# Optimization experiments

Measured on AMD Instinct MI355X. Metric: run time of the kernel, lower is better.

Reference implementation:

```python
import jax, jax.numpy as jnp
import numpy as np

N = 16384      # number of nodes (= in_num_dim)
F_DIM = 512    # node feature dim (= in_node_dim)
EMBED = 128    # embed_dim (D1)
OUT = 64       # out_dim (final latent)
E = 524288     # number of edges (avg degree 32)
GAT_SLOPE = 0.5    # GATConv negative_slope
LRELU_SLOPE = 0.01 # F.leaky_relu default on embed


def setup_inputs() -> dict:
    key = jax.random.key(0)
    ks = jax.random.split(key, 10)
    x = jax.random.normal(ks[0], (N, F_DIM), dtype=jnp.float32)
    edge_index = jax.random.randint(ks[1], (2, E), 0, N, dtype=jnp.int64)
    adj = jnp.zeros((1,), dtype=jnp.float32)  # unused by forward (as in source)
    # GATConv params (single head)
    W_gat = jax.random.normal(ks[2], (F_DIM, OUT), dtype=jnp.float32) / np.sqrt(F_DIM)
    att_src = jax.random.normal(ks[3], (OUT,), dtype=jnp.float32) * 0.1
    att_dst = jax.random.normal(ks[4], (OUT,), dtype=jnp.float32) * 0.1
    b_gat = jnp.zeros((OUT,), dtype=jnp.float32)
    # AttributeAE params: dense1 (N -> EMBED), dense2 (EMBED -> OUT)
    W1 = jax.random.normal(ks[5], (N, EMBED), dtype=jnp.float32) / np.sqrt(N)
    b1 = jnp.zeros((EMBED,), dtype=jnp.float32)
    W2 = jax.random.normal(ks[6], (EMBED, OUT), dtype=jnp.float32) / np.sqrt(EMBED)
    b2 = jnp.zeros((OUT,), dtype=jnp.float32)
    return dict(x=x, edge_index=edge_index, adj=adj, W_gat=W_gat,
                att_src=att_src, att_dst=att_dst, b_gat=b_gat,
                W1=W1, b1=b1, W2=W2, b2=b2)


def _gat_conv(x, edge_index, W_gat, att_src, att_dst, b_gat):
    # PyG GATConv, heads=1, with self-loops appended.
    n = x.shape[0]
    loops = jnp.arange(n, dtype=edge_index.dtype)
    src = jnp.concatenate([edge_index[0], loops])  # message sources j
    dst = jnp.concatenate([edge_index[1], loops])  # aggregation targets i
    h = x @ W_gat                                  # [N, OUT]
    a_src = h @ att_src                            # [N]
    a_dst = h @ att_dst                            # [N]
    e = jax.nn.leaky_relu(a_src[src] + a_dst[dst], GAT_SLOPE)  # [E+N]
    # segment softmax over incoming edges of each dst node
    m = jax.ops.segment_max(e, dst, num_segments=n)
    p = jnp.exp(e - m[dst])
    denom = jax.ops.segment_sum(p, dst, num_segments=n)
    alpha = p / denom[dst]
    out = jax.ops.segment_sum(alpha[:, None] * h[src], dst, num_segments=n)
    return out + b_gat


def _forward(x, edge_index, W_gat, att_src, att_dst, b_gat, W1, b1, W2, b2):
    # StructureAE
    embed_x = jax.nn.leaky_relu(
        _gat_conv(x, edge_index, W_gat, att_src, att_dst, b_gat), LRELU_SLOPE)
    A_hat = jax.nn.sigmoid(embed_x @ embed_x.T)          # [N, N]
    # AttributeAE (dropout = 0 -> identity)
    h1 = jax.nn.relu(x.T @ W1 + b1)                      # [F, EMBED]
    h2 = h1 @ W2 + b2                                    # [F, OUT]
    X_hat = embed_x @ h2.T                               # [N, F]
    return A_hat, X_hat


def reference(x, edge_index, adj, W_gat, att_src, att_dst, b_gat, W1, b1, W2, b2):
    # adj is accepted but unused, matching the torch forward signature
    return _forward(x, edge_index, W_gat, att_src, att_dst, b_gat, W1, b1, W2, b2)
```

## Files before the change

### kernel.cpp

```cpp
#include <hip/hip_runtime.h>
#include <hip/hip_bf16.h>

#define NN 16384
#define FD 512
#define EMB 128
#define OD 64
#define NE 524288

typedef __bf16 bf16x8 __attribute__((ext_vector_type(8)));
typedef float f32x4 __attribute__((ext_vector_type(4)));
typedef unsigned short u16;

__device__ inline float bfu2f(u16 u) {
    unsigned int x = (unsigned int)u << 16;
    float f;
    __builtin_memcpy(&f, &x, 4);
    return f;
}

__global__ __launch_bounds__(256) void k_prep(
    const float* __restrict__ x, __hip_bfloat16* __restrict__ xbf,
    const float* __restrict__ Wg, __hip_bfloat16* __restrict__ WgT,
    const int* __restrict__ ei, int* __restrict__ deg,
    const float* __restrict__ W1, float* __restrict__ part) {
    __shared__ float xs[4][64];
    __shared__ float wsh[4][EMB];
    int b = blockIdx.x;
    int t = threadIdx.x;
    if (b < 256) {
        int fb = b & 7, nc = b >> 3;
        int f0 = fb * 64, nb = nc * 512;
        int eb = (t & 15) * 8;
        int fbase = (t >> 4) * 4;
        float acc[4][8] = {};
        for (int n4 = 0; n4 < 512; n4 += 4) {
            { int nn = t >> 6, ff = t & 63;
              xs[nn][ff] = x[(size_t)(nb + n4 + nn) * FD + f0 + ff]; }
#pragma unroll
            for (int j = 0; j < 2; ++j) {
                int idx = t + j * 256;
                wsh[idx >> 7][idx & 127] = W1[(size_t)(nb + n4 + (idx >> 7)) * EMB + (idx & 127)];
            }
            __syncthreads();
#pragma unroll
            for (int nn = 0; nn < 4; ++nn) {
                float xv[4], wv[8];
#pragma unroll
                for (int i = 0; i < 4; ++i) xv[i] = xs[nn][fbase + i];
#pragma unroll
                for (int j = 0; j < 8; ++j) wv[j] = wsh[nn][eb + j];
#pragma unroll
                for (int i = 0; i < 4; ++i)
#pragma unroll
                    for (int j = 0; j < 8; ++j) acc[i][j] += xv[i] * wv[j];
            }
            __syncthreads();
        }
#pragma unroll
        for (int i = 0; i < 4; ++i) {
            float* dst = &part[((size_t)nc * FD + f0 + fbase + i) * EMB + eb];
            *reinterpret_cast<f32x4*>(dst) = *reinterpret_cast<f32x4*>(&acc[i][0]);
            *reinterpret_cast<f32x4*>(dst + 4) = *reinterpret_cast<f32x4*>(&acc[i][4]);
        }
        return;
    }
    b -= 256;
    if (b < NE / 256) {
        int i = b * 256 + t;
        atomicAdd(deg + ei[NE + i], 1);
        return;
    }
    b -= NE / 256;
    if (b < NN * FD / 2048) {
        size_t i = ((size_t)b * 256 + t) * 8;
        float4 v0 = *reinterpret_cast<const float4*>(x + i);
        float4 v1 = *reinterpret_cast<const float4*>(x + i + 4);
        __hip_bfloat16 o[8];
        o[0] = __float2bfloat16(v0.x); o[1] = __float2bfloat16(v0.y);
        o[2] = __float2bfloat16(v0.z); o[3] = __float2bfloat16(v0.w);
        o[4] = __float2bfloat16(v1.x); o[5] = __float2bfloat16(v1.y);
        o[6] = __float2bfloat16(v1.z); o[7] = __float2bfloat16(v1.w);
        *reinterpret_cast<uint4*>(xbf + i) = *reinterpret_cast<const uint4*>(o);
        return;
    }
    b -= NN * FD / 2048;
    {
        int c = t >> 2;
        int k0 = (t & 3) * 128;
        for (int j = 0; j < 128; ++j)
            WgT[c * 512 + k0 + j] = __float2bfloat16(Wg[(size_t)(k0 + j) * OD + c]);
    }
}

__global__ __launch_bounds__(256) void k_scan(const int* __restrict__ deg,
                                              int* __restrict__ row_start) {
    __shared__ int part[256];
    int t = threadIdx.x;
    int base = t * 64;
    int s = 0;
    for (int j = 0; j < 64; ++j) s += deg[base + j];
    part[t] = s;
    __syncthreads();
    for (int off = 1; off < 256; off <<= 1) {
        int v = (t >= off) ? part[t - off] : 0;
        __syncthreads();
        part[t] += v;
        __syncthreads();
    }
    int run = part[t] - s;
    if (t == 255) row_start[NN] = part[255];
    for (int j = 0; j < 64; ++j) { row_start[base + j] = run; run += deg[base + j]; }
}

__global__ __launch_bounds__(256) void k_mid(
    const int* __restrict__ ei, const int* __restrict__ row_start,
    int* __restrict__ cursor, int* __restrict__ ssrc,
    const __hip_bfloat16* __restrict__ xbf, const __hip_bfloat16* __restrict__ WgT,
    const float* __restrict__ att_s, const float* __restrict__ att_d,
    __hip_bfloat16* __restrict__ hbf, float* __restrict__ a_src, float* __restrict__ a_dst,
    const float* __restrict__ part, const float* __restrict__ b1,
    const float* __restrict__ W2, const float* __restrict__ b2,
    __hip_bfloat16* __restrict__ h2bf) {
    __shared__ float hv[4][EMB];
    int b = blockIdx.x;
    int t = threadIdx.x;
    if (b < NE / 256) {
        int i = b * 256 + t;
        int d = ei[NE + i];
        int pos = atomicAdd(cursor + d, 1);
        ssrc[row_start[d] + pos] = ei[i];
        return;
    }
    b -= NE / 256;
    int w = t >> 6, l = t & 63;
    if (b < NN / 64) {
        int lg = l >> 4, lm = l & 15;
        int r0 = b * 64 + w * 16;
        const bf16x8* Xp = reinterpret_cast<const bf16x8*>(xbf);
        const bf16x8* Wp = reinterpret_cast<const bf16x8*>(WgT);
        bf16x8 a[16];
        size_t abase = (size_t)(r0 + lm) * 64 + lg;
#pragma unroll
        for (int kc = 0; kc < 16; ++kc) a[kc] = Xp[abase + kc * 4];
        f32x4 acc[4];
#pragma unroll
        for (int j = 0; j < 4; ++j) {
            f32x4 c = {0.f, 0.f, 0.f, 0.f};
            size_t bbase = (size_t)(j * 16 + lm) * 64 + lg;
#pragma unroll
            for (int kc = 0; kc < 16; ++kc)
                c = __builtin_amdgcn_mfma_f32_16x16x32_bf16(a[kc], Wp[bbase + kc * 4], c, 0, 0, 0);
            acc[j] = c;
        }
#pragma unroll
        for (int j = 0; j < 4; ++j)
#pragma unroll
            for (int reg = 0; reg < 4; ++reg)
                hbf[(size_t)(r0 + lg * 4 + reg) * OD + j * 16 + lm] = __float2bfloat16(acc[j][reg]);
        float ats0 = att_s[lm], ats1 = att_s[16 + lm], ats2 = att_s[32 + lm], ats3 = att_s[48 + lm];
        float atd0 = att_d[lm], atd1 = att_d[16 + lm], atd2 = att_d[32 + lm], atd3 = att_d[48 + lm];
#pragma unroll
        for (int reg = 0; reg < 4; ++reg) {
            float ps = acc[0][reg] * ats0 + acc[1][reg] * ats1 + acc[2][reg] * ats2 + acc[3][reg] * ats3;
            float pd = acc[0][reg] * atd0 + acc[1][reg] * atd1 + acc[2][reg] * atd2 + acc[3][reg] * atd3;
#pragma unroll
            for (int off = 1; off < 16; off <<= 1) {
                ps += __shfl_xor(ps, off, 64);
                pd += __shfl_xor(pd, off, 64);
            }
            if (lm == 0) {
                int r = r0 + lg * 4 + reg;
                a_src[r] = ps;
                a_dst[r] = pd;
            }
        }
        return;
    }
    b -= NN / 64;
    {
        int f = b * 4 + w;
        float s0 = 0.f, s1 = 0.f;
        for (int nc = 0; nc < 32; ++nc) {
            const float* p = part + ((size_t)nc * FD + f) * EMB;
            s0 += p[l];
            s1 += p[l + 64];
        }
        s0 += b1[l]; s1 += b1[l + 64];
        hv[w][l] = s0 > 0.f ? s0 : 0.f;
        hv[w][l + 64] = s1 > 0.f ? s1 : 0.f;
        __syncthreads();
        float acc = b2[l];
        const float* myhv = hv[w];
        for (int e = 0; e < EMB; ++e)
            acc += myhv[e] * W2[e * OD + l];
        h2bf[(size_t)f * OD + l] = __float2bfloat16(acc);
    }
}

__global__ __launch_bounds__(256) void k_aggcsr(
    const int* __restrict__ row_start, const int* __restrict__ ssrc,
    const float* __restrict__ a_src, const float* __restrict__ a_dst,
    const u16* __restrict__ hb, const float* __restrict__ bg,
    __hip_bfloat16* __restrict__ ebf) {
    int node = blockIdx.x * 4 + (threadIdx.x >> 6);
    int lane = threadIdx.x & 63;
    float ad = a_dst[node];
    float e0 = a_src[node] + ad;
    e0 = e0 > 0.f ? e0 : 0.5f * e0;
    float p0 = __expf(e0);
    float denom = p0;
    float acc = p0 * bfu2f(hb[(size_t)node * OD + lane]);
    int j0 = row_start[node], j1 = row_start[node + 1];
    int j = j0;
    for (; j + 2 <= j1; j += 2) {
        int sA = ssrc[j], sB = ssrc[j + 1];
        float hA = bfu2f(hb[(size_t)sA * OD + lane]);
        float hB = bfu2f(hb[(size_t)sB * OD + lane]);
        float eA = a_src[sA] + ad, eB = a_src[sB] + ad;
        eA = eA > 0.f ? eA : 0.5f * eA;
        eB = eB > 0.f ? eB : 0.5f * eB;
        float pA = __expf(eA), pB = __expf(eB);
        denom += pA + pB;
        acc += pA * hA + pB * hB;
    }
    if (j < j1) {
        int s = ssrc[j];
        float e = a_src[s] + ad;
        e = e > 0.f ? e : 0.5f * e;
        float pv = __expf(e);
        denom += pv;
        acc += pv * bfu2f(hb[(size_t)s * OD + lane]);
    }
    float v = acc * __builtin_amdgcn_rcpf(denom) + bg[lane];
    v = v > 0.f ? v : 0.01f * v;
    ebf[(size_t)node * OD + lane] = __float2bfloat16(v);
}

template <bool SIG>
__device__ __forceinline__ void mmT_body(const __hip_bfloat16* __restrict__ A,
                                         const __hip_bfloat16* __restrict__ B,
                                         float* __restrict__ out, int ldo,
                                         int rowT, int colT) {
    __shared__ float ls[4][32 * 68];
    int w = threadIdx.x >> 6, l = threadIdx.x & 63;
    int lg = l >> 4, lm = l & 15;
    int i0 = rowT * 128 + w * 32;
    int j0 = colT * 128;
    const bf16x8* Ap = reinterpret_cast<const bf16x8*>(A);
    const bf16x8* Bp = reinterpret_cast<const bf16x8*>(B);
    size_t arow = (size_t)(i0 + lm) * 8;
    bf16x8 a0 = Ap[arow + lg];
    bf16x8 a1 = Ap[arow + 4 + lg];
    bf16x8 a2 = Ap[arow + 128 + lg];
    bf16x8 a3 = Ap[arow + 128 + 4 + lg];
    f32x4 accL[8], accH[8];
#pragma unroll
    for (int ct = 0; ct < 8; ++ct) {
        size_t brow = (size_t)(j0 + ct * 16 + lm) * 8;
        bf16x8 b0 = Bp[brow + lg];
        bf16x8 b1 = Bp[brow + 4 + lg];
        f32x4 cL = {0.f, 0.f, 0.f, 0.f};
        f32x4 cH = {0.f, 0.f, 0.f, 0.f};
        cL = __builtin_amdgcn_mfma_f32_16x16x32_bf16(a0, b0, cL, 0, 0, 0);
        cL = __builtin_amdgcn_mfma_f32_16x16x32_bf16(a1, b1, cL, 0, 0, 0);
        cH = __builtin_amdgcn_mfma_f32_16x16x32_bf16(a2, b0, cH, 0, 0, 0);
        cH = __builtin_amdgcn_mfma_f32_16x16x32_bf16(a3, b1, cH, 0, 0, 0);
        accL[ct] = cL;
        accH[ct] = cH;
    }
    float* myl = ls[w];
#pragma unroll
    for (int ph = 0; ph < 2; ++ph) {
        if (ph == 1) {
            asm volatile("s_waitcnt lgkmcnt(0)" ::: "memory");
            __builtin_amdgcn_sched_barrier(0);
        }
#pragma unroll
        for (int c4 = 0; c4 < 4; ++c4) {
            int ct = ph * 4 + c4;
            int col = c4 * 16 + lm;
#pragma unroll
            for (int reg = 0; reg < 4; ++reg) {
                float vL = accL[ct][reg], vH = accH[ct][reg];
                if (SIG) {
                    vL = __builtin_amdgcn_rcpf(1.f + __expf(-vL));
                    vH = __builtin_amdgcn_rcpf(1.f + __expf(-vH));
                }
                int row = lg * 4 + reg;
                myl[row * 68 + col] = vL;
                myl[(row + 16) * 68 + col] = vH;
            }
        }
        asm volatile("s_waitcnt lgkmcnt(0)" ::: "memory");
        __builtin_amdgcn_sched_barrier(0);
#pragma unroll
        for (int i = 0; i < 8; ++i) {
            int row = i * 4 + lg;
            f32x4 v = *reinterpret_cast<const f32x4*>(&myl[row * 68 + lm * 4]);
            float* dst = &out[(size_t)(i0 + row) * ldo + j0 + ph * 64 + lm * 4];
            __builtin_nontemporal_store(v, reinterpret_cast<f32x4*>(dst));
        }
    }
}

__global__ __launch_bounds__(256) void k_mmX(const __hip_bfloat16* __restrict__ A,
                                             const __hip_bfloat16* __restrict__ B,
                                             float* __restrict__ out) {
    mmT_body<false>(A, B, out, FD, blockIdx.y, blockIdx.x);
}

__global__ __launch_bounds__(256) void k_mmA(const __hip_bfloat16* __restrict__ A,
                                             float* __restrict__ out) {
    mmT_body<true>(A, A, out, NN, blockIdx.y, blockIdx.x);
}

extern "C" void kernel_launch(void* const* d_in, const int* in_sizes, int n_in,
                              void* d_out, int out_size, void* d_ws, size_t ws_size,
                              hipStream_t stream) {
    const float* x     = (const float*)d_in[0];
    const int*   ei    = (const int*)d_in[1];
    const float* Wg    = (const float*)d_in[3];
    const float* att_s = (const float*)d_in[4];
    const float* att_d = (const float*)d_in[5];
    const float* bg    = (const float*)d_in[6];
    const float* W1    = (const float*)d_in[7];
    const float* b1    = (const float*)d_in[8];
    const float* W2    = (const float*)d_in[9];
    const float* b2    = (const float*)d_in[10];

    float* ws    = (float*)d_ws;
    float* a_src = ws;
    float* a_dst = a_src + NN;
    int*   deg   = (int*)(a_dst + NN);
    int*   cursor= deg + NN;
    int*   row_start = cursor + NN;
    int*   ssrc  = row_start + NN + 4;
    float* part  = (float*)(ssrc + NE);
    __hip_bfloat16* xbf  = (__hip_bfloat16*)(part + 32 * FD * EMB);
    __hip_bfloat16* WgT  = xbf + (size_t)NN * FD;
    __hip_bfloat16* hbf  = WgT + (size_t)OD * FD;
    __hip_bfloat16* ebf  = hbf + (size_t)NN * OD;
    __hip_bfloat16* h2bf = ebf + (size_t)NN * OD;

    float* Ahat = (float*)d_out;
    float* Xhat = Ahat + (size_t)NN * NN;

    hipMemsetAsync(deg, 0, 2 * NN * sizeof(int), stream);
    const int prep_blocks = 256 + NE / 256 + NN * FD / 2048 + 1;
    k_prep<<<prep_blocks, 256, 0, stream>>>(x, xbf, Wg, WgT, ei, deg, W1, part);
    k_scan<<<1, 256, 0, stream>>>(deg, row_start);
    const int mid_blocks = NE / 256 + NN / 64 + FD / 4;
    k_mid<<<mid_blocks, 256, 0, stream>>>(ei, row_start, cursor, ssrc,
                                          xbf, WgT, att_s, att_d,
                                          hbf, a_src, a_dst,
                                          part, b1, W2, b2, h2bf);
    k_aggcsr<<<NN / 4, 256, 0, stream>>>(row_start, ssrc, a_src, a_dst,
                                         (const u16*)hbf, bg, ebf);
    k_mmX<<<dim3(FD / 128, NN / 128), 256, 0, stream>>>(ebf, h2bf, Xhat);
    k_mmA<<<dim3(NN / 128, NN / 128), 256, 0, stream>>>(ebf, Ahat);
}
```

Baseline: 409.1 us.

## Restructure A_hat kernel into persistent row-strip blocks writing full rows

Rewrites the sigmoid(E·Eᵀ) kernel so that each block owns a 32-row strip and loops over all 16384 columns in 512-wide chunks, rather than launching a 2D grid of 128x128 tiles. Each wave keeps its A fragment in registers and writes 16 full rows of 256 contiguous floats per step through a wider LDS staging buffer. This gives longer contiguous nontemporal store streams and fewer, longer-lived blocks (512 total). The catch is less latency hiding: the B loads and stores within each loop iteration are serialized, and there are fewer blocks in flight. k_mmX is inlined from the old template with no functional change.

```diff
diff --git a/kernel.cpp b/kernel.cpp
--- a/kernel.cpp
+++ b/kernel.cpp
@@ -236,16 +236,14 @@
     ebf[(size_t)node * OD + lane] = __float2bfloat16(v);
 }
 
-template <bool SIG>
-__device__ __forceinline__ void mmT_body(const __hip_bfloat16* __restrict__ A,
-                                         const __hip_bfloat16* __restrict__ B,
-                                         float* __restrict__ out, int ldo,
-                                         int rowT, int colT) {
+__global__ __launch_bounds__(256) void k_mmX(const __hip_bfloat16* __restrict__ A,
+                                             const __hip_bfloat16* __restrict__ B,
+                                             float* __restrict__ out) {
     __shared__ float ls[4][32 * 68];
     int w = threadIdx.x >> 6, l = threadIdx.x & 63;
     int lg = l >> 4, lm = l & 15;
-    int i0 = rowT * 128 + w * 32;
-    int j0 = colT * 128;
+    int i0 = blockIdx.y * 128 + w * 32;
+    int j0 = blockIdx.x * 128;
     const bf16x8* Ap = reinterpret_cast<const bf16x8*>(A);
     const bf16x8* Bp = reinterpret_cast<const bf16x8*>(B);
     size_t arow = (size_t)(i0 + lm) * 8;
@@ -271,24 +269,15 @@
     float* myl = ls[w];
 #pragma unroll
     for (int ph = 0; ph < 2; ++ph) {
-        if (ph == 1) {
-            asm volatile("s_waitcnt lgkmcnt(0)" ::: "memory");
-            __builtin_amdgcn_sched_barrier(0);
-        }
 #pragma unroll
         for (int c4 = 0; c4 < 4; ++c4) {
             int ct = ph * 4 + c4;
             int col = c4 * 16 + lm;
 #pragma unroll
             for (int reg = 0; reg < 4; ++reg) {
-                float vL = accL[ct][reg], vH = accH[ct][reg];
-                if (SIG) {
-                    vL = __builtin_amdgcn_rcpf(1.f + __expf(-vL));
-                    vH = __builtin_amdgcn_rcpf(1.f + __expf(-vH));
-                }
                 int row = lg * 4 + reg;
-                myl[row * 68 + col] = vL;
-                myl[(row + 16) * 68 + col] = vH;
+                myl[row * 68 + col] = accL[ct][reg];
+                myl[(row + 16) * 68 + col] = accH[ct][reg];
             }
         }
         asm volatile("s_waitcnt lgkmcnt(0)" ::: "memory");
@@ -297,21 +286,58 @@
         for (int i = 0; i < 8; ++i) {
             int row = i * 4 + lg;
             f32x4 v = *reinterpret_cast<const f32x4*>(&myl[row * 68 + lm * 4]);
-            float* dst = &out[(size_t)(i0 + row) * ldo + j0 + ph * 64 + lm * 4];
+            float* dst = &out[(size_t)(i0 + row) * FD + j0 + ph * 64 + lm * 4];
             __builtin_nontemporal_store(v, reinterpret_cast<f32x4*>(dst));
         }
     }
-}
-
-__global__ __launch_bounds__(256) void k_mmX(const __hip_bfloat16* __restrict__ A,
-                                             const __hip_bfloat16* __restrict__ B,
-                                             float* __restrict__ out) {
-    mmT_body<false>(A, B, out, FD, blockIdx.y, blockIdx.x);
 }
 
 __global__ __launch_bounds__(256) void k_mmA(const __hip_bfloat16* __restrict__ A,
                                              float* __restrict__ out) {
-    mmT_body<true>(A, A, out, NN, blockIdx.y, blockIdx.x);
+    __shared__ float ls[4][16 * 260];
+    int w = threadIdx.x >> 6, l = threadIdx.x & 63;
+    int lg = l >> 4, lm = l & 15;
+    int rg = (w >> 1) * 16;
+    int ch = (w & 1) * 256;
+    int r0 = blockIdx.x * 32 + rg;
+    const bf16x8* Ap = reinterpret_cast<const bf16x8*>(A);
+    size_t arow = (size_t)(r0 + lm) * 8;
+    bf16x8 a0 = Ap[arow + lg];
+    bf16x8 a1 = Ap[arow + 4 + lg];
+    float* myl = ls[w];
+#pragma unroll 1
+    for (int tcol = 0; tcol < NN; tcol += 512) {
+        int j0 = tcol + ch;
+        f32x4 acc[16];
+#pragma unroll
+        for (int ct = 0; ct < 16; ++ct) {
+            size_t brow = (size_t)(j0 + ct * 16 + lm) * 8;
+            bf16x8 b0 = Ap[brow + lg];
+            bf16x8 b1 = Ap[brow + 4 + lg];
+            f32x4 c = {0.f, 0.f, 0.f, 0.f};
+            c = __builtin_amdgcn_mfma_f32_16x16x32_bf16(a0, b0, c, 0, 0, 0);
+            c = __builtin_amdgcn_mfma_f32_16x16x32_bf16(a1, b1, c, 0, 0, 0);
+            acc[ct] = c;
+        }
+#pragma unroll
+        for (int ct = 0; ct < 16; ++ct) {
+            int col = ct * 16 + lm;
+#pragma unroll
+            for (int reg = 0; reg < 4; ++reg) {
+                float v = acc[ct][reg];
+                v = __builtin_amdgcn_rcpf(1.f + __expf(-v));
+                myl[(lg * 4 + reg) * 260 + col] = v;
+            }
+        }
+        asm volatile("s_waitcnt lgkmcnt(0)" ::: "memory");
+        __builtin_amdgcn_sched_barrier(0);
+#pragma unroll
+        for (int i = 0; i < 16; ++i) {
+            f32x4 v = *reinterpret_cast<const f32x4*>(&myl[i * 260 + l * 4]);
+            float* dst = &out[(size_t)(r0 + i) * NN + j0 + l * 4];
+            __builtin_nontemporal_store(v, reinterpret_cast<f32x4*>(dst));
+        }
+    }
 }
 
 extern "C" void kernel_launch(void* const* d_in, const int* in_sizes, int n_in,
@@ -357,5 +383,5 @@
     k_aggcsr<<<NN / 4, 256, 0, stream>>>(row_start, ssrc, a_src, a_dst,
                                          (const u16*)hbf, bg, ebf);
     k_mmX<<<dim3(FD / 128, NN / 128), 256, 0, stream>>>(ebf, h2bf, Xhat);
-    k_mmA<<<dim3(NN / 128, NN / 128), 256, 0, stream>>>(ebf, Ahat);
-}
+    k_mmA<<<NN / 32, 256, 0, stream>>>(ebf, Ahat);
+}
```

After: 487.8 us. 1.19x slower.
